# Kernel tuning notes

Hardware: AMD Instinct MI355X
Metric: run time of the kernel (lower is better)

The kernel has to match this reference:

```python
import jax, jax.numpy as jnp
import numpy as np

DIM = 128
HID = 128


def setup_inputs() -> dict:
    key = jax.random.key(0)
    ks = jax.random.split(key, 7)
    x = jax.random.normal(ks[0], (1, 256, 512, DIM), dtype=jnp.float32)
    s = 1.0 / np.sqrt(DIM)
    return {
        "x": x,
        "ln_g": jnp.ones((DIM,), jnp.float32),
        "ln_b": jnp.zeros((DIM,), jnp.float32),
        "w_left": jax.random.normal(ks[1], (DIM, HID), jnp.float32) * s,
        "b_left": jnp.zeros((HID,), jnp.float32),
        "w_right": jax.random.normal(ks[2], (DIM, HID), jnp.float32) * s,
        "b_right": jnp.zeros((HID,), jnp.float32),
        "w_out": jax.random.normal(ks[3], (HID, DIM), jnp.float32) * (1.0 / np.sqrt(HID)),
        "b_out": jnp.zeros((DIM,), jnp.float32),
    }


def reference(x, ln_g, ln_b, w_left, b_left, w_right, b_right, w_out, b_out):
    # LayerNorm over last dim (eps matches torch default 1e-5)
    mu = jnp.mean(x, axis=-1, keepdims=True)
    var = jnp.mean(jnp.square(x - mu), axis=-1, keepdims=True)
    xn = (x - mu) * jax.lax.rsqrt(var + 1e-5) * ln_g + ln_b
    # dual projections: (b, m, i, h)
    left = jnp.einsum('bmid,dh->bmih', xn, w_left) + b_left
    right = jnp.einsum('bmjd,dh->bmjh', xn, w_right) + b_right
    # mean over m of (left_i + right_j) == mean_m(left)_i + mean_m(right)_j
    # (exact algebraic identity; avoids the (b,m,i,j,h) intermediate)
    left_m = jnp.mean(left, axis=1)   # (b, i, h)
    right_m = jnp.mean(right, axis=1)  # (b, j, h)
    outer = left_m[:, :, None, :] + right_m[:, None, :, :]  # (b, i, j, h)
    return jnp.einsum('bijh,hd->bijd', outer, w_out) + b_out
```

## Files before the change

kernel.cpp:

```cpp
#include <hip/hip_runtime.h>
#include <hip/hip_bf16.h>


#define DIM 128
#define NI  512
#define NM  256

__global__ __launch_bounds__(512) void ln_mean_kernel(
    const float* __restrict__ x,
    const float* __restrict__ ln_g,
    const float* __restrict__ ln_b,
    float* __restrict__ S)
{
    const int i    = blockIdx.x;
    const int tid  = threadIdx.x;
    const int lane = tid & 63;
    const int wave = tid >> 6;

    const float g0  = ln_g[2*lane];
    const float g1  = ln_g[2*lane + 1];
    const float be0 = ln_b[2*lane];
    const float be1 = ln_b[2*lane + 1];

    float acc0 = 0.f, acc1 = 0.f;

    #pragma unroll 4
    for (int t = 0; t < NM/8; ++t) {
        const int m = wave + (t << 3);
        const float2 v = *(const float2*)(x + (((size_t)(m * NI + i)) << 7) + 2*lane);

        float s  = v.x + v.y;
        float s2 = v.x*v.x + v.y*v.y;
        #pragma unroll
        for (int off = 32; off; off >>= 1) {
            s  += __shfl_xor(s,  off);
            s2 += __shfl_xor(s2, off);
        }
        const float mu   = s * (1.f/128.f);
        const float var  = s2 * (1.f/128.f) - mu*mu;
        const float rstd = rsqrtf(var + 1e-5f);

        acc0 += (v.x - mu) * rstd * g0 + be0;
        acc1 += (v.y - mu) * rstd * g1 + be1;
    }

    __shared__ float red0[512];
    __shared__ float red1[512];
    red0[tid] = acc0;
    red1[tid] = acc1;
    __syncthreads();

    if (tid < 64) {
        float a0 = 0.f, a1 = 0.f;
        #pragma unroll
        for (int w = 0; w < 8; ++w) {
            a0 += red0[(w << 6) + tid];
            a1 += red1[(w << 6) + tid];
        }
        float2 r;
        r.x = a0 * (1.f/(float)NM);
        r.y = a1 * (1.f/(float)NM);
        *(float2*)(S + ((size_t)i << 7) + 2*tid) = r;
    }
}

__global__ __launch_bounds__(256) void project_kernel(
    const float* __restrict__ S,
    const float* __restrict__ w_left,  const float* __restrict__ b_left,
    const float* __restrict__ w_right, const float* __restrict__ b_right,
    const float* __restrict__ w_out,   const float* __restrict__ b_out,
    float* __restrict__ L, float* __restrict__ R)
{
    const int i   = blockIdx.x;
    const int tid = threadIdx.x;
    const int h   = tid & 127;
    const bool isR = (tid >= 128);

    __shared__ float sS[128];
    __shared__ float sTL[128];
    __shared__ float sTR[128];

    if (tid < 128) sS[tid] = S[((size_t)i << 7) + tid];
    __syncthreads();

    const float* W = isR ? w_right : w_left;
    float acc = isR ? b_right[h] : b_left[h];
    #pragma unroll 8
    for (int d = 0; d < DIM; ++d) {
        acc += sS[d] * W[(d << 7) + h];
    }
    (isR ? sTR : sTL)[h] = acc;
    __syncthreads();

    const float* T = isR ? sTR : sTL;
    float acc2 = isR ? b_out[h] : 0.f;
    #pragma unroll 8
    for (int hh = 0; hh < DIM; ++hh) {
        acc2 += T[hh] * w_out[(hh << 7) + h];
    }
    (isR ? R : L)[((size_t)i << 7) + h] = acc2;
}

__global__ __launch_bounds__(256) void expand_kernel(
    const float4* __restrict__ L4,
    const float4* __restrict__ R4,
    float4* __restrict__ out4)
{
    const size_t t = (size_t)blockIdx.x * 256 + threadIdx.x;
    const int d4 = (int)(t & 31);
    const int j  = (int)((t >> 5) & 511);
    const int i  = (int)(t >> 14);

    const float4 a = L4[(i << 5) + d4];
    const float4 b = R4[(j << 5) + d4];
    float4 o;
    o.x = a.x + b.x;
    o.y = a.y + b.y;
    o.z = a.z + b.z;
    o.w = a.w + b.w;
    out4[t] = o;
}

extern "C" void kernel_launch(void* const* d_in, const int* in_sizes, int n_in,
                              void* d_out, int out_size, void* d_ws, size_t ws_size,
                              hipStream_t stream) {
    const float* x       = (const float*)d_in[0];
    const float* ln_g    = (const float*)d_in[1];
    const float* ln_b    = (const float*)d_in[2];
    const float* w_left  = (const float*)d_in[3];
    const float* b_left  = (const float*)d_in[4];
    const float* w_right = (const float*)d_in[5];
    const float* b_right = (const float*)d_in[6];
    const float* w_out   = (const float*)d_in[7];
    const float* b_out   = (const float*)d_in[8];

    float* S = (float*)d_ws;
    float* L = S + NI * DIM;
    float* R = L + NI * DIM;

    ln_mean_kernel<<<NI, 512, 0, stream>>>(x, ln_g, ln_b, S);
    project_kernel<<<NI, 256, 0, stream>>>(S, w_left, b_left, w_right, b_right,
                                           w_out, b_out, L, R);

    const int total4 = NI * NI * (DIM / 4);
    expand_kernel<<<total4 / 256, 256, 0, stream>>>((const float4*)L,
                                                    (const float4*)R,
                                                    (float4*)d_out);
}
```

Measured before the change: 212.0 us.

## Fuse layernorm-mean with projections and restructure expand with nontemporal stores

Merges the layernorm+mean kernel and the projection kernel into one launch, so there is one fewer launch and no round trip of the intermediate S through global memory. The x reads are widened to float4 with nontemporal loads, and each half-wave now handles a separate row. The expand kernel has each thread loop over 16 j rows while reusing its L vector, and writes the 128MB output with nontemporal stores to avoid cache pollution. In exchange, the projection step inside the fused kernel runs on only half the threads of a 512-thread block.

```diff
diff --git a/kernel.cpp b/kernel.cpp
--- a/kernel.cpp
+++ b/kernel.cpp
@@ -1,38 +1,42 @@
 #include <hip/hip_runtime.h>
-#include <hip/hip_bf16.h>
 
 
 #define DIM 128
 #define NI  512
 #define NM  256
 
-__global__ __launch_bounds__(512) void ln_mean_kernel(
+typedef float f32x4 __attribute__((ext_vector_type(4)));
+
+__global__ __launch_bounds__(512) void ln_mean_project_kernel(
     const float* __restrict__ x,
-    const float* __restrict__ ln_g,
-    const float* __restrict__ ln_b,
-    float* __restrict__ S)
+    const float* __restrict__ ln_g,    const float* __restrict__ ln_b,
+    const float* __restrict__ w_left,  const float* __restrict__ b_left,
+    const float* __restrict__ w_right, const float* __restrict__ b_right,
+    const float* __restrict__ w_out,   const float* __restrict__ b_out,
+    float* __restrict__ L, float* __restrict__ R)
 {
     const int i    = blockIdx.x;
     const int tid  = threadIdx.x;
     const int lane = tid & 63;
     const int wave = tid >> 6;
+    const int l31  = lane & 31;
+    const int half = lane >> 5;
 
-    const float g0  = ln_g[2*lane];
-    const float g1  = ln_g[2*lane + 1];
-    const float be0 = ln_b[2*lane];
-    const float be1 = ln_b[2*lane + 1];
+    const float4 g4 = ((const float4*)ln_g)[l31];
+    const float4 b4 = ((const float4*)ln_b)[l31];
 
-    float acc0 = 0.f, acc1 = 0.f;
+    float4 acc = make_float4(0.f, 0.f, 0.f, 0.f);
 
     #pragma unroll 4
-    for (int t = 0; t < NM/8; ++t) {
-        const int m = wave + (t << 3);
-        const float2 v = *(const float2*)(x + (((size_t)(m * NI + i)) << 7) + 2*lane);
+    for (int t = 0; t < NM/16; ++t) {
+        const int m = (t << 4) + (wave << 1) + half;
+        const f32x4 v = __builtin_nontemporal_load(
+            (const f32x4*)(x + (((size_t)(m * NI + i)) << 7)) + l31);
 
-        float s  = v.x + v.y;
-        float s2 = v.x*v.x + v.y*v.y;
+        float s  = v.x + v.y + v.z + v.w;
+        float s2 = v.x*v.x + v.y*v.y + v.z*v.z + v.w*v.w;
         #pragma unroll
-        for (int off = 32; off; off >>= 1) {
+        for (int off = 16; off; off >>= 1) {
             s  += __shfl_xor(s,  off);
             s2 += __shfl_xor(s2, off);
         }
@@ -40,85 +44,80 @@
         const float var  = s2 * (1.f/128.f) - mu*mu;
         const float rstd = rsqrtf(var + 1e-5f);
 
-        acc0 += (v.x - mu) * rstd * g0 + be0;
-        acc1 += (v.y - mu) * rstd * g1 + be1;
+        acc.x += (v.x - mu) * rstd * g4.x + b4.x;
+        acc.y += (v.y - mu) * rstd * g4.y + b4.y;
+        acc.z += (v.z - mu) * rstd * g4.z + b4.z;
+        acc.w += (v.w - mu) * rstd * g4.w + b4.w;
     }
 
-    __shared__ float red0[512];
-    __shared__ float red1[512];
-    red0[tid] = acc0;
-    red1[tid] = acc1;
+    __shared__ float4 red[512];
+    __shared__ float  sS[128];
+    __shared__ float  sT[256];
+
+    red[tid] = acc;
     __syncthreads();
 
-    if (tid < 64) {
-        float a0 = 0.f, a1 = 0.f;
+    if (tid < 32) {
+        float4 a = make_float4(0.f, 0.f, 0.f, 0.f);
         #pragma unroll
-        for (int w = 0; w < 8; ++w) {
-            a0 += red0[(w << 6) + tid];
-            a1 += red1[(w << 6) + tid];
+        for (int g = 0; g < 16; ++g) {
+            const float4 r = red[(g << 5) + tid];
+            a.x += r.x; a.y += r.y; a.z += r.z; a.w += r.w;
         }
-        float2 r;
-        r.x = a0 * (1.f/(float)NM);
-        r.y = a1 * (1.f/(float)NM);
-        *(float2*)(S + ((size_t)i << 7) + 2*tid) = r;
+        sS[4*tid+0] = a.x * (1.f/(float)NM);
+        sS[4*tid+1] = a.y * (1.f/(float)NM);
+        sS[4*tid+2] = a.z * (1.f/(float)NM);
+        sS[4*tid+3] = a.w * (1.f/(float)NM);
+    }
+    __syncthreads();
+
+    if (tid < 256) {
+        const int  h   = tid & 127;
+        const bool isR = tid >= 128;
+        const float* W = isR ? w_right : w_left;
+        float a = isR ? b_right[h] : b_left[h];
+        #pragma unroll 8
+        for (int d = 0; d < DIM; ++d)
+            a += sS[d] * W[(d << 7) + h];
+        sT[tid] = a;
+    }
+    __syncthreads();
+
+    if (tid < 256) {
+        const int  h   = tid & 127;
+        const bool isR = tid >= 128;
+        const float* T = sT + (isR ? 128 : 0);
+        float a = isR ? b_out[h] : 0.f;
+        #pragma unroll 8
+        for (int hh = 0; hh < DIM; ++hh)
+            a += T[hh] * w_out[(hh << 7) + h];
+        (isR ? R : L)[((size_t)i << 7) + h] = a;
     }
 }
 
-__global__ __launch_bounds__(256) void project_kernel(
-    const float* __restrict__ S,
-    const float* __restrict__ w_left,  const float* __restrict__ b_left,
-    const float* __restrict__ w_right, const float* __restrict__ b_right,
-    const float* __restrict__ w_out,   const float* __restrict__ b_out,
-    float* __restrict__ L, float* __restrict__ R)
+__global__ __launch_bounds__(256) void expand_kernel(
+    const f32x4* __restrict__ L4,
+    const f32x4* __restrict__ R4,
+    f32x4* __restrict__ out4)
 {
-    const int i   = blockIdx.x;
+    const int b   = blockIdx.x;
+    const int i   = b >> 2;
+    const int jq  = (b & 3) << 7;
     const int tid = threadIdx.x;
-    const int h   = tid & 127;
-    const bool isR = (tid >= 128);
+    const int d4  = tid & 31;
+    const int jl  = tid >> 5;
 
-    __shared__ float sS[128];
-    __shared__ float sTL[128];
-    __shared__ float sTR[128];
+    const f32x4 a = L4[(i << 5) + d4];
 
-    if (tid < 128) sS[tid] = S[((size_t)i << 7) + tid];
-    __syncthreads();
+    const f32x4* rp = R4   + ((size_t)(jq + jl)          << 5) + d4;
+    f32x4*       op = out4 + ((size_t)(i * NI + jq + jl) << 5) + d4;
 
-    const float* W = isR ? w_right : w_left;
-    float acc = isR ? b_right[h] : b_left[h];
-    #pragma unroll 8
-    for (int d = 0; d < DIM; ++d) {
-        acc += sS[d] * W[(d << 7) + h];
+    #pragma unroll 4
+    for (int t = 0; t < 16; ++t) {
+        const f32x4 rv = rp[(size_t)t << 8];
+        const f32x4 o  = a + rv;
+        __builtin_nontemporal_store(o, op + ((size_t)t << 8));
     }
-    (isR ? sTR : sTL)[h] = acc;
-    __syncthreads();
-
-    const float* T = isR ? sTR : sTL;
-    float acc2 = isR ? b_out[h] : 0.f;
-    #pragma unroll 8
-    for (int hh = 0; hh < DIM; ++hh) {
-        acc2 += T[hh] * w_out[(hh << 7) + h];
-    }
-    (isR ? R : L)[((size_t)i << 7) + h] = acc2;
-}
-
-__global__ __launch_bounds__(256) void expand_kernel(
-    const float4* __restrict__ L4,
-    const float4* __restrict__ R4,
-    float4* __restrict__ out4)
-{
-    const size_t t = (size_t)blockIdx.x * 256 + threadIdx.x;
-    const int d4 = (int)(t & 31);
-    const int j  = (int)((t >> 5) & 511);
-    const int i  = (int)(t >> 14);
-
-    const float4 a = L4[(i << 5) + d4];
-    const float4 b = R4[(j << 5) + d4];
-    float4 o;
-    o.x = a.x + b.x;
-    o.y = a.y + b.y;
-    o.z = a.z + b.z;
-    o.w = a.w + b.w;
-    out4[t] = o;
 }
 
 extern "C" void kernel_launch(void* const* d_in, const int* in_sizes, int n_in,
@@ -134,16 +133,13 @@
     const float* w_out   = (const float*)d_in[7];
     const float* b_out   = (const float*)d_in[8];
 
-    float* S = (float*)d_ws;
-    float* L = S + NI * DIM;
+    float* L = (float*)d_ws;
     float* R = L + NI * DIM;
 
-    ln_mean_kernel<<<NI, 512, 0, stream>>>(x, ln_g, ln_b, S);
-    project_kernel<<<NI, 256, 0, stream>>>(S, w_left, b_left, w_right, b_right,
-                                           w_out, b_out, L, R);
+    ln_mean_project_kernel<<<NI, 512, 0, stream>>>(
+        x, ln_g, ln_b, w_left, b_left, w_right, b_right, w_out, b_out, L, R);
 
-    const int total4 = NI * NI * (DIM / 4);
-    expand_kernel<<<total4 / 256, 256, 0, stream>>>((const float4*)L,
-                                                    (const float4*)R,
-                                                    (float4*)d_out);
+    expand_kernel<<<2048, 256, 0, stream>>>((const f32x4*)L,
+                                            (const f32x4*)R,
+                                            (f32x4*)d_out);
 }
```

New measurement: 208.6 us. No clear change (-1.6%).
